# Kernel optimization log

Measured on AMD Instinct MI355X. Metric: run time of the kernel, lower is better.

## Reference

```python
import jax, jax.numpy as jnp
import numpy as np

N, F_IN, HID, C, E = 100000, 1024, 16, 64, 3200000
BN_EPS = 1e-5


def setup_inputs() -> dict:
    key = jax.random.key(0)
    ks = jax.random.split(key, 8)
    x = jax.random.normal(ks[0], (N, F_IN), jnp.float32)
    edge_index = jax.random.randint(ks[1], (2, E), 0, N, dtype=jnp.int32)
    w1 = jax.random.normal(ks[2], (F_IN, HID), jnp.float32) / np.float32(np.sqrt(F_IN))
    b1 = jnp.zeros((HID,), jnp.float32)
    w2 = jax.random.normal(ks[3], (HID, C), jnp.float32) / np.float32(np.sqrt(HID))
    b2 = jnp.zeros((C,), jnp.float32)
    mlp_w = jax.random.normal(ks[4], (C, C), jnp.float32) / np.float32(np.sqrt(C))
    mlp_b = jnp.zeros((C,), jnp.float32)
    bn_gamma = jnp.ones((C,), jnp.float32)
    bn_beta = jnp.zeros((C,), jnp.float32)
    # per-node channel weight param, xavier_normal_ init on shape (N, 1)
    xavier_std = np.float32(np.sqrt(2.0 / (N + 1)))
    weight_raw = jax.random.normal(ks[5], (N, 1), jnp.float32) * xavier_std
    return {"x": x, "edge_index": edge_index, "w1": w1, "b1": b1, "w2": w2,
            "b2": b2, "mlp_w": mlp_w, "mlp_b": mlp_b, "bn_gamma": bn_gamma,
            "bn_beta": bn_beta, "weight_raw": weight_raw}


def _gcn_norm(edge_index, n):
    # PyG GCNConv default: add self-loops, norm = deg^-1/2[src] * deg^-1/2[dst]
    loop = jnp.arange(n, dtype=edge_index.dtype)
    src = jnp.concatenate([edge_index[0], loop])
    dst = jnp.concatenate([edge_index[1], loop])
    deg = jax.ops.segment_sum(jnp.ones_like(dst, dtype=jnp.float32), dst, num_segments=n)
    dis = jax.lax.rsqrt(jnp.maximum(deg, 1.0))  # deg >= 1 with self-loops
    norm = dis[src] * dis[dst]
    return src, dst, norm


def _gcn_conv(h, src, dst, norm, w, b, n):
    h = h @ w                              # [N, out] dense transform first
    msg = h[src] * norm[:, None]           # gather + scale per edge
    out = jax.ops.segment_sum(msg, dst, num_segments=n)  # scatter-add
    return out + b


def reference(x, edge_index, w1, b1, w2, b2, mlp_w, mlp_b, bn_gamma, bn_beta, weight_raw):
    n = x.shape[0]
    src, dst, norm = _gcn_norm(edge_index, n)
    h = _gcn_conv(x, src, dst, norm, w1, b1, n)
    h = jax.nn.relu(h)                     # dropout is identity in eval mode
    h = _gcn_conv(h, src, dst, norm, w2, b2, n)
    h = jax.nn.log_softmax(h, axis=1)
    h = jnp.exp(weight_raw) * h            # exp(xavier param) channel weight
    h = h @ mlp_w + mlp_b                  # final MLP (C*1 -> C)
    mean = jnp.mean(h, axis=0)
    var = jnp.mean(jnp.square(h - mean), axis=0)  # biased var, BN training stats
    h = (h - mean) * jax.lax.rsqrt(var + BN_EPS) * bn_gamma + bn_beta
    return jax.nn.log_softmax(h, axis=1)
```

## Files before the change

### kernel.cpp

```cpp
#include <hip/hip_runtime.h>
#include <math.h>

#define NN   100000
#define FIN  1024
#define HIDN 16
#define CCH  64
#define EE   3200000
#define BNEPS 1e-5f
#define NB   ((NN + 255) / 256)
#define NPART 8
#define PSZ  (NN / NPART)

__global__ __launch_bounds__(256) void k_hist(const int* __restrict__ ei,
                                              unsigned* __restrict__ deg) {
  int p = blockIdx.x & 7;
  int blk = blockIdx.x >> 3;
  int nblk = gridDim.x >> 3;
  int lo = p * PSZ, hi = lo + PSZ;
  for (int e = blk * 256 + threadIdx.x; e < EE; e += nblk * 256) {
    int d = ei[EE + e];
    if (d >= lo && d < hi) atomicAdd(&deg[d], 1u);
  }
}

__global__ __launch_bounds__(256) void k_scan_part(const unsigned* __restrict__ deg,
                                                   unsigned* __restrict__ exc,
                                                   unsigned* __restrict__ bsum) {
  __shared__ unsigned s[256];
  int t = threadIdx.x, i = blockIdx.x * 256 + t;
  unsigned v = (i < NN) ? deg[i] : 0u;
  s[t] = v;
  __syncthreads();
#pragma unroll
  for (int off = 1; off < 256; off <<= 1) {
    unsigned u = (t >= off) ? s[t - off] : 0u;
    __syncthreads();
    s[t] += u;
    __syncthreads();
  }
  if (i < NN) exc[i] = s[t] - v;
  if (t == 255) bsum[blockIdx.x] = s[255];
}

__global__ __launch_bounds__(512) void k_scan_boff(const unsigned* __restrict__ bsum,
                                                   unsigned* __restrict__ boff) {
  __shared__ unsigned s[512];
  int t = threadIdx.x;
  unsigned v = (t < NB) ? bsum[t] : 0u;
  s[t] = v;
  __syncthreads();
#pragma unroll
  for (int off = 1; off < 512; off <<= 1) {
    unsigned u = (t >= off) ? s[t - off] : 0u;
    __syncthreads();
    s[t] += u;
    __syncthreads();
  }
  if (t < NB) boff[t] = s[t] - v;
}

__global__ __launch_bounds__(256) void k_scan_final(const unsigned* __restrict__ exc,
                                                    const unsigned* __restrict__ boff,
                                                    const unsigned* __restrict__ deg,
                                                    int* __restrict__ rowptr,
                                                    int* __restrict__ cur,
                                                    float* __restrict__ dis) {
  int i = blockIdx.x * 256 + threadIdx.x;
  if (i < NN) {
    int r = (int)(boff[i >> 8] + exc[i]);
    rowptr[i] = r;
    cur[i] = r;
    dis[i] = rsqrtf((float)(deg[i] + 1u));
  } else if (i == NN) {
    rowptr[NN] = EE;
  }
}

__global__ __launch_bounds__(256) void k_place(const int* __restrict__ ei,
                                               int* __restrict__ cur,
                                               int* __restrict__ perm) {
  int p = blockIdx.x & 7;
  int blk = blockIdx.x >> 3;
  int nblk = gridDim.x >> 3;
  int lo = p * PSZ, hi = lo + PSZ;
  for (int e = blk * 256 + threadIdx.x; e < EE; e += nblk * 256) {
    int d = ei[EE + e];
    if (d >= lo && d < hi) {
      int s = ei[e];
      int slot = atomicAdd(&cur[d], 1);
      perm[slot] = s;
    }
  }
}

#define G1_ROWS_PER_BLOCK 128
__global__ __launch_bounds__(256, 2) void k_gemm1(const float* __restrict__ x,
                                                  const float* __restrict__ w1,
                                                  const float* __restrict__ dis,
                                                  float* __restrict__ xw1s) {
  __shared__ __align__(16) float w1s[1024 * 16];
  const float4* w1v = (const float4*)w1;
  for (int idx = threadIdx.x; idx < 4096; idx += 256) {
    int k = idx >> 2, qj = idx & 3;
    int pq = qj ^ ((k >> 1) & 3);
    *(float4*)&w1s[(k << 4) + (pq << 2)] = w1v[idx];
  }
  __syncthreads();

  const int lane = threadIdx.x & 63;
  const int wave = threadIdx.x >> 6;
  const int sw = (lane >> 1) & 3;
  const int wave_row0 = blockIdx.x * G1_ROWS_PER_BLOCK + wave * 32;

  for (int g = 0; g < 8; ++g) {
    int row0 = wave_row0 + g * 4;
    if (row0 >= NN) break;
    int r0 = row0;
    int r1 = min(row0 + 1, NN - 1);
    int r2 = min(row0 + 2, NN - 1);
    int r3 = min(row0 + 3, NN - 1);

    const float* p0 = x + (size_t)r0 * FIN + lane;
    const float* p1 = x + (size_t)r1 * FIN + lane;
    const float* p2 = x + (size_t)r2 * FIN + lane;
    const float* p3 = x + (size_t)r3 * FIN + lane;

    float xa[16], xb[16], xc[16], xd[16];
#pragma unroll
    for (int i = 0; i < 16; ++i) {
      xa[i] = p0[i * 64];
      xb[i] = p1[i * 64];
      xc[i] = p2[i * 64];
      xd[i] = p3[i * 64];
    }

    float acc[64];
#pragma unroll
    for (int t = 0; t < 64; ++t) acc[t] = 0.0f;

#pragma unroll
    for (int i = 0; i < 16; ++i) {
      const float* wr = &w1s[(i * 64 + lane) << 4];
      float xv0 = xa[i], xv1 = xb[i], xv2 = xc[i], xv3 = xd[i];
#pragma unroll
      for (int q = 0; q < 4; ++q) {
        float4 wq = *(const float4*)(wr + ((q ^ sw) << 2));
        int b = q * 4;
        acc[b + 0]      += xv0 * wq.x;
        acc[b + 1]      += xv0 * wq.y;
        acc[b + 2]      += xv0 * wq.z;
        acc[b + 3]      += xv0 * wq.w;
        acc[16 + b + 0] += xv1 * wq.x;
        acc[16 + b + 1] += xv1 * wq.y;
        acc[16 + b + 2] += xv1 * wq.z;
        acc[16 + b + 3] += xv1 * wq.w;
        acc[32 + b + 0] += xv2 * wq.x;
        acc[32 + b + 1] += xv2 * wq.y;
        acc[32 + b + 2] += xv2 * wq.z;
        acc[32 + b + 3] += xv2 * wq.w;
        acc[48 + b + 0] += xv3 * wq.x;
        acc[48 + b + 1] += xv3 * wq.y;
        acc[48 + b + 2] += xv3 * wq.z;
        acc[48 + b + 3] += xv3 * wq.w;
      }
    }

#pragma unroll
    for (int o = 32; o >= 1; o >>= 1) {
      bool up = (lane & o) != 0;
#pragma unroll
      for (int t = 0; t < o; ++t) {
        float send = up ? acc[t] : acc[t + o];
        float recv = __shfl_xor(send, o, 64);
        float keep = up ? acc[t + o] : acc[t];
        acc[t] = keep + recv;
      }
    }

    int r = lane >> 4, j = lane & 15;
    int grow = row0 + r;
    if (grow < NN) xw1s[grow * HIDN + j] = acc[0] * dis[grow];
  }
}

template <int MODE>
__global__ __launch_bounds__(256) void k_agg(const int* __restrict__ rowptr,
                                             const int* __restrict__ perm,
                                             const float* __restrict__ dis,
                                             const float* __restrict__ sfs,
                                             const float* __restrict__ b1,
                                             float* __restrict__ out) {
  int g = blockIdx.x * 4 + (threadIdx.x >> 6);
  if (g >= NN) return;
  int lane = threadIdx.x & 63;
  int eo = lane >> 4;
  int j = lane & 15;
  int beg = rowptr[g], end = rowptr[g + 1];
  float acc = 0.0f;
  for (int e = beg + eo; e < end; e += 4) {
    int s = perm[e];
    acc += sfs[(size_t)s * HIDN + j];
  }
  acc += __shfl_xor(acc, 16, 64);
  acc += __shfl_xor(acc, 32, 64);
  if (eo == 0) {
    float di = dis[g];
    float v = di * (acc + sfs[(size_t)g * HIDN + j]);
    if (MODE == 0)
      out[(size_t)g * HIDN + j] = fmaxf(v + b1[j], 0.0f) * di;
    else
      out[(size_t)g * HIDN + j] = v;
  }
}

__global__ __launch_bounds__(256) void k_fuse2(const float* __restrict__ agg2,
                                               const float* __restrict__ w2,
                                               const float* __restrict__ b2,
                                               const float* __restrict__ mlpw,
                                               const float* __restrict__ mlpb,
                                               const float* __restrict__ wraw,
                                               float* __restrict__ out,
                                               double* __restrict__ gsum,
                                               double* __restrict__ gsq) {
  __shared__ float w2s[HIDN * CCH];
  __shared__ float mlps[CCH * CCH];
  __shared__ double reds[256];
  __shared__ double redq[256];
  for (int idx = threadIdx.x; idx < HIDN * CCH; idx += 256) w2s[idx] = w2[idx];
  for (int idx = threadIdx.x; idx < CCH * CCH; idx += 256) mlps[idx] = mlpw[idx];
  __syncthreads();

  const int lane = threadIdx.x & 63;
  const int wave = threadIdx.x >> 6;
  const int j = lane;
  const float b2j = b2[j];
  const float mbj = mlpb[j];
  const int gw = blockIdx.x * 4 + wave;
  const int nw = gridDim.x * 4;

  double sum = 0.0, sq = 0.0;
  for (int i = gw; i < NN; i += nw) {
    float av = agg2[(size_t)i * HIDN + (lane & 15)];
    float h2 = b2j;
#pragma unroll
    for (int k = 0; k < HIDN; ++k)
      h2 = fmaf(__shfl(av, k, 64), w2s[k * CCH + j], h2);

    float mx = h2;
#pragma unroll
    for (int o = 32; o >= 1; o >>= 1) mx = fmaxf(mx, __shfl_xor(mx, o, 64));
    float ex = __expf(h2 - mx);
    float se = ex;
#pragma unroll
    for (int o = 32; o >= 1; o >>= 1) se += __shfl_xor(se, o, 64);
    float lsm = h2 - mx - __logf(se);

    float g = __expf(wraw[i]) * lsm;

    float m = mbj;
#pragma unroll
    for (int c = 0; c < CCH; ++c)
      m = fmaf(__shfl(g, c, 64), mlps[c * CCH + j], m);

    out[(size_t)i * CCH + j] = m;
    sum += (double)m;
    sq = fma((double)m, (double)m, sq);
  }

  reds[threadIdx.x] = sum;
  redq[threadIdx.x] = sq;
  __syncthreads();
  if (threadIdx.x < 64) {
    double s = reds[threadIdx.x] + reds[threadIdx.x + 64] +
               reds[threadIdx.x + 128] + reds[threadIdx.x + 192];
    double q = redq[threadIdx.x] + redq[threadIdx.x + 64] +
               redq[threadIdx.x + 128] + redq[threadIdx.x + 192];
    atomicAdd(&gsum[threadIdx.x], s);
    atomicAdd(&gsq[threadIdx.x], q);
  }
}

__global__ void k_stats(const double* __restrict__ gsum,
                        const double* __restrict__ gsq,
                        const float* __restrict__ gamma,
                        const float* __restrict__ beta,
                        float* __restrict__ bnp) {
  int j = threadIdx.x;
  if (j >= CCH) return;
  const double inv_n = 1.0 / (double)NN;
  double mean = gsum[j] * inv_n;
  double var = gsq[j] * inv_n - mean * mean;
  float sc = (float)(rsqrt(var + (double)BNEPS)) * gamma[j];
  bnp[j] = (float)mean;
  bnp[CCH + j] = sc;
  bnp[2 * CCH + j] = beta[j];
}

__global__ __launch_bounds__(256) void k_out(float* __restrict__ out,
                                             const float* __restrict__ bnp) {
  const int lane = threadIdx.x & 63;
  const int wave = threadIdx.x >> 6;
  const int j = lane;
  const float mean = bnp[j];
  const float sc = bnp[CCH + j];
  const float bt = bnp[2 * CCH + j];
  const int gw = blockIdx.x * 4 + wave;
  const int nw = gridDim.x * 4;
  for (int i = gw; i < NN; i += nw) {
    float m = out[(size_t)i * CCH + j];
    float y = fmaf(m - mean, sc, bt);
    float mx = y;
#pragma unroll
    for (int o = 32; o >= 1; o >>= 1) mx = fmaxf(mx, __shfl_xor(mx, o, 64));
    float ex = __expf(y - mx);
    float se = ex;
#pragma unroll
    for (int o = 32; o >= 1; o >>= 1) se += __shfl_xor(se, o, 64);
    out[(size_t)i * CCH + j] = y - mx - __logf(se);
  }
}

extern "C" void kernel_launch(void* const* d_in, const int* in_sizes, int n_in,
                              void* d_out, int out_size, void* d_ws, size_t ws_size,
                              hipStream_t stream) {
  const float* x     = (const float*)d_in[0];
  const int*   ei    = (const int*)d_in[1];
  const float* w1    = (const float*)d_in[2];
  const float* b1    = (const float*)d_in[3];
  const float* w2    = (const float*)d_in[4];
  const float* b2    = (const float*)d_in[5];
  const float* mlpw  = (const float*)d_in[6];
  const float* mlpb  = (const float*)d_in[7];
  const float* gamma = (const float*)d_in[8];
  const float* beta  = (const float*)d_in[9];
  const float* wraw  = (const float*)d_in[10];
  float* out = (float*)d_out;

  char* w = (char*)d_ws;
  size_t off = 0;
  auto take = [&](size_t bytes) -> void* {
    void* p = w + off;
    off = (off + bytes + 255) & ~(size_t)255;
    return p;
  };
  unsigned* deg    = (unsigned*)take((size_t)NN * 4);
  float*    dis    = (float*)take((size_t)NN * 4);
  unsigned* exc    = (unsigned*)take((size_t)NN * 4);
  unsigned* bsum   = (unsigned*)take((size_t)NB * 4);
  unsigned* boff   = (unsigned*)take((size_t)NB * 4);
  int*      rowptr = (int*)take((size_t)(NN + 1) * 4);
  int*      cur    = (int*)take((size_t)NN * 4);
  int*      perm   = (int*)take((size_t)EE * 4);
  float*    xw1s   = (float*)take((size_t)NN * HIDN * 4);
  float*    rh1s   = (float*)take((size_t)NN * HIDN * 4);
  float*    agg2   = (float*)take((size_t)NN * HIDN * 4);
  double*   gsum   = (double*)take(CCH * 8);
  double*   gsq    = (double*)take(CCH * 8);
  float*    bnp    = (float*)take(3 * CCH * 4);
  (void)ws_size; (void)n_in; (void)in_sizes; (void)out_size;

  hipMemsetAsync(deg, 0, (size_t)NN * 4, stream);
  hipMemsetAsync(gsum, 0, CCH * 8, stream);
  hipMemsetAsync(gsq, 0, CCH * 8, stream);

  k_hist<<<2048, 256, 0, stream>>>(ei, deg);
  k_scan_part<<<NB, 256, 0, stream>>>(deg, exc, bsum);
  k_scan_boff<<<1, 512, 0, stream>>>(bsum, boff);
  k_scan_final<<<(NN + 256) / 256 + 1, 256, 0, stream>>>(exc, boff, deg, rowptr, cur, dis);
  k_place<<<2048, 256, 0, stream>>>(ei, cur, perm);

  k_gemm1<<<(NN + G1_ROWS_PER_BLOCK - 1) / G1_ROWS_PER_BLOCK, 256, 0, stream>>>(
      x, w1, dis, xw1s);
  k_agg<0><<<(NN + 3) / 4, 256, 0, stream>>>(rowptr, perm, dis, xw1s, b1, rh1s);
  k_agg<1><<<(NN + 3) / 4, 256, 0, stream>>>(rowptr, perm, dis, rh1s, b1, agg2);
  k_fuse2<<<2048, 256, 0, stream>>>(agg2, w2, b2, mlpw, mlpb, wraw, out, gsum, gsq);
  k_stats<<<1, 64, 0, stream>>>(gsum, gsq, gamma, beta, bnp);
  k_out<<<1024, 256, 0, stream>>>(out, bnp);
}
```

Baseline: 701.3 us.

## Double-buffer x loads in gemm1, unroll aggregation, use LDS broadcast in fuse2

The first GEMM kernel now double-buffers its x row loads in registers, so the next 4-row group is fetched while the current one is computed. The aggregation kernel keeps two accumulators per lane so that two independent gathers are in flight. The fused second stage replaces per-element wave shuffles with LDS broadcast reads of packed float2 weights. The extra 64-float buffer raises register pressure in gemm1, which may spill or cut occupancy. In fuse2, per-wave LDS buffers are written and read without an explicit barrier and rely on wave-synchronous execution.

```diff
diff --git a/kernel.cpp b/kernel.cpp
--- a/kernel.cpp
+++ b/kernel.cpp
@@ -94,6 +94,78 @@
 }
 
 #define G1_ROWS_PER_BLOCK 128
+
+__device__ __forceinline__ void g1_load(const float* __restrict__ x, int row0,
+                                        int lane, float (&buf)[64]) {
+  int r0 = min(row0,     NN - 1);
+  int r1 = min(row0 + 1, NN - 1);
+  int r2 = min(row0 + 2, NN - 1);
+  int r3 = min(row0 + 3, NN - 1);
+  const float* p0 = x + (size_t)r0 * FIN + lane;
+  const float* p1 = x + (size_t)r1 * FIN + lane;
+  const float* p2 = x + (size_t)r2 * FIN + lane;
+  const float* p3 = x + (size_t)r3 * FIN + lane;
+#pragma unroll
+  for (int i = 0; i < 16; ++i) {
+    buf[i]      = p0[i * 64];
+    buf[16 + i] = p1[i * 64];
+    buf[32 + i] = p2[i * 64];
+    buf[48 + i] = p3[i * 64];
+  }
+}
+
+__device__ __forceinline__ void g1_compute_store(const float (&buf)[64],
+                                                 const float* w1s, int row0,
+                                                 int lane, int sw,
+                                                 const float* __restrict__ dis,
+                                                 float* __restrict__ xw1s) {
+  float acc[64];
+#pragma unroll
+  for (int t = 0; t < 64; ++t) acc[t] = 0.0f;
+
+#pragma unroll
+  for (int i = 0; i < 16; ++i) {
+    const float* wr = &w1s[(i * 64 + lane) << 4];
+    float xv0 = buf[i], xv1 = buf[16 + i], xv2 = buf[32 + i], xv3 = buf[48 + i];
+#pragma unroll
+    for (int q = 0; q < 4; ++q) {
+      float4 wq = *(const float4*)(wr + ((q ^ sw) << 2));
+      int b = q * 4;
+      acc[b + 0]      += xv0 * wq.x;
+      acc[b + 1]      += xv0 * wq.y;
+      acc[b + 2]      += xv0 * wq.z;
+      acc[b + 3]      += xv0 * wq.w;
+      acc[16 + b + 0] += xv1 * wq.x;
+      acc[16 + b + 1] += xv1 * wq.y;
+      acc[16 + b + 2] += xv1 * wq.z;
+      acc[16 + b + 3] += xv1 * wq.w;
+      acc[32 + b + 0] += xv2 * wq.x;
+      acc[32 + b + 1] += xv2 * wq.y;
+      acc[32 + b + 2] += xv2 * wq.z;
+      acc[32 + b + 3] += xv2 * wq.w;
+      acc[48 + b + 0] += xv3 * wq.x;
+      acc[48 + b + 1] += xv3 * wq.y;
+      acc[48 + b + 2] += xv3 * wq.z;
+      acc[48 + b + 3] += xv3 * wq.w;
+    }
+  }
+
+#pragma unroll
+  for (int o = 32; o >= 1; o >>= 1) {
+    bool up = (lane & o) != 0;
+#pragma unroll
+    for (int t = 0; t < o; ++t) {
+      float send = up ? acc[t] : acc[t + o];
+      float recv = __shfl_xor(send, o, 64);
+      float keep = up ? acc[t + o] : acc[t];
+      acc[t] = keep + recv;
+    }
+  }
+
+  int grow = row0 + (lane >> 4);
+  if (grow < NN) xw1s[grow * HIDN + (lane & 15)] = acc[0] * dis[grow];
+}
+
 __global__ __launch_bounds__(256, 2) void k_gemm1(const float* __restrict__ x,
                                                   const float* __restrict__ w1,
                                                   const float* __restrict__ dis,
@@ -112,74 +184,16 @@
   const int sw = (lane >> 1) & 3;
   const int wave_row0 = blockIdx.x * G1_ROWS_PER_BLOCK + wave * 32;
 
-  for (int g = 0; g < 8; ++g) {
-    int row0 = wave_row0 + g * 4;
-    if (row0 >= NN) break;
-    int r0 = row0;
-    int r1 = min(row0 + 1, NN - 1);
-    int r2 = min(row0 + 2, NN - 1);
-    int r3 = min(row0 + 3, NN - 1);
-
-    const float* p0 = x + (size_t)r0 * FIN + lane;
-    const float* p1 = x + (size_t)r1 * FIN + lane;
-    const float* p2 = x + (size_t)r2 * FIN + lane;
-    const float* p3 = x + (size_t)r3 * FIN + lane;
-
-    float xa[16], xb[16], xc[16], xd[16];
-#pragma unroll
-    for (int i = 0; i < 16; ++i) {
-      xa[i] = p0[i * 64];
-      xb[i] = p1[i * 64];
-      xc[i] = p2[i * 64];
-      xd[i] = p3[i * 64];
-    }
-
-    float acc[64];
-#pragma unroll
-    for (int t = 0; t < 64; ++t) acc[t] = 0.0f;
-
-#pragma unroll
-    for (int i = 0; i < 16; ++i) {
-      const float* wr = &w1s[(i * 64 + lane) << 4];
-      float xv0 = xa[i], xv1 = xb[i], xv2 = xc[i], xv3 = xd[i];
-#pragma unroll
-      for (int q = 0; q < 4; ++q) {
-        float4 wq = *(const float4*)(wr + ((q ^ sw) << 2));
-        int b = q * 4;
-        acc[b + 0]      += xv0 * wq.x;
-        acc[b + 1]      += xv0 * wq.y;
-        acc[b + 2]      += xv0 * wq.z;
-        acc[b + 3]      += xv0 * wq.w;
-        acc[16 + b + 0] += xv1 * wq.x;
-        acc[16 + b + 1] += xv1 * wq.y;
-        acc[16 + b + 2] += xv1 * wq.z;
-        acc[16 + b + 3] += xv1 * wq.w;
-        acc[32 + b + 0] += xv2 * wq.x;
-        acc[32 + b + 1] += xv2 * wq.y;
-        acc[32 + b + 2] += xv2 * wq.z;
-        acc[32 + b + 3] += xv2 * wq.w;
-        acc[48 + b + 0] += xv3 * wq.x;
-        acc[48 + b + 1] += xv3 * wq.y;
-        acc[48 + b + 2] += xv3 * wq.z;
-        acc[48 + b + 3] += xv3 * wq.w;
-      }
-    }
-
-#pragma unroll
-    for (int o = 32; o >= 1; o >>= 1) {
-      bool up = (lane & o) != 0;
-#pragma unroll
-      for (int t = 0; t < o; ++t) {
-        float send = up ? acc[t] : acc[t + o];
-        float recv = __shfl_xor(send, o, 64);
-        float keep = up ? acc[t + o] : acc[t];
-        acc[t] = keep + recv;
-      }
-    }
-
-    int r = lane >> 4, j = lane & 15;
-    int grow = row0 + r;
-    if (grow < NN) xw1s[grow * HIDN + j] = acc[0] * dis[grow];
+  float bufA[64], bufB[64];
+  g1_load(x, wave_row0, lane, bufA);
+
+  for (int gg = 0; gg < 4; ++gg) {
+    int r_even = wave_row0 + (2 * gg) * 4;
+    int r_odd  = wave_row0 + (2 * gg + 1) * 4;
+    g1_load(x, r_odd, lane, bufB);
+    g1_compute_store(bufA, w1s, r_even, lane, sw, dis, xw1s);
+    if (gg < 3) g1_load(x, wave_row0 + (2 * gg + 2) * 4, lane, bufA);
+    g1_compute_store(bufB, w1s, r_odd, lane, sw, dis, xw1s);
   }
 }
 
@@ -196,11 +210,16 @@
   int eo = lane >> 4;
   int j = lane & 15;
   int beg = rowptr[g], end = rowptr[g + 1];
-  float acc = 0.0f;
-  for (int e = beg + eo; e < end; e += 4) {
-    int s = perm[e];
-    acc += sfs[(size_t)s * HIDN + j];
-  }
+  float acc0 = 0.0f, acc1 = 0.0f;
+  int e = beg + eo;
+  for (; e + 4 < end; e += 8) {
+    int s0 = perm[e];
+    int s1 = perm[e + 4];
+    acc0 += sfs[(size_t)s0 * HIDN + j];
+    acc1 += sfs[(size_t)s1 * HIDN + j];
+  }
+  if (e < end) acc0 += sfs[(size_t)perm[e] * HIDN + j];
+  float acc = acc0 + acc1;
   acc += __shfl_xor(acc, 16, 64);
   acc += __shfl_xor(acc, 32, 64);
   if (eo == 0) {
@@ -222,12 +241,20 @@
                                                float* __restrict__ out,
                                                double* __restrict__ gsum,
                                                double* __restrict__ gsq) {
-  __shared__ float w2s[HIDN * CCH];
-  __shared__ float mlps[CCH * CCH];
+  __shared__ __align__(16) float2 w2p[8 * CCH];
+  __shared__ __align__(16) float2 mlpp[32 * CCH];
+  __shared__ __align__(16) float avbuf[4][HIDN];
+  __shared__ __align__(16) float gbuf[4][CCH];
   __shared__ double reds[256];
   __shared__ double redq[256];
-  for (int idx = threadIdx.x; idx < HIDN * CCH; idx += 256) w2s[idx] = w2[idx];
-  for (int idx = threadIdx.x; idx < CCH * CCH; idx += 256) mlps[idx] = mlpw[idx];
+  for (int idx = threadIdx.x; idx < 8 * CCH; idx += 256) {
+    int k2 = idx >> 6, j = idx & 63;
+    w2p[idx] = make_float2(w2[(2 * k2) * CCH + j], w2[(2 * k2 + 1) * CCH + j]);
+  }
+  for (int idx = threadIdx.x; idx < 32 * CCH; idx += 256) {
+    int c2 = idx >> 6, j = idx & 63;
+    mlpp[idx] = make_float2(mlpw[(2 * c2) * CCH + j], mlpw[(2 * c2 + 1) * CCH + j]);
+  }
   __syncthreads();
 
   const int lane = threadIdx.x & 63;
@@ -241,10 +268,17 @@
   double sum = 0.0, sq = 0.0;
   for (int i = gw; i < NN; i += nw) {
     float av = agg2[(size_t)i * HIDN + (lane & 15)];
-    float h2 = b2j;
-#pragma unroll
-    for (int k = 0; k < HIDN; ++k)
-      h2 = fmaf(__shfl(av, k, 64), w2s[k * CCH + j], h2);
+    if (lane < HIDN) avbuf[wave][lane] = av;
+
+    float2 h2p = make_float2(0.0f, 0.0f);
+#pragma unroll
+    for (int k2 = 0; k2 < 8; ++k2) {
+      float2 a = *(const float2*)&avbuf[wave][2 * k2];
+      float2 wv = w2p[k2 * CCH + j];
+      h2p.x = fmaf(a.x, wv.x, h2p.x);
+      h2p.y = fmaf(a.y, wv.y, h2p.y);
+    }
+    float h2 = h2p.x + h2p.y + b2j;
 
     float mx = h2;
 #pragma unroll
@@ -255,12 +289,18 @@
     for (int o = 32; o >= 1; o >>= 1) se += __shfl_xor(se, o, 64);
     float lsm = h2 - mx - __logf(se);
 
-    float g = __expf(wraw[i]) * lsm;
-
-    float m = mbj;
-#pragma unroll
-    for (int c = 0; c < CCH; ++c)
-      m = fmaf(__shfl(g, c, 64), mlps[c * CCH + j], m);
+    float gg = __expf(wraw[i]) * lsm;
+    gbuf[wave][j] = gg;
+
+    float2 mp = make_float2(0.0f, 0.0f);
+#pragma unroll
+    for (int c2 = 0; c2 < 32; ++c2) {
+      float2 gv = *(const float2*)&gbuf[wave][2 * c2];
+      float2 wv = mlpp[c2 * CCH + j];
+      mp.x = fmaf(gv.x, wv.x, mp.x);
+      mp.y = fmaf(gv.y, wv.y, mp.y);
+    }
+    float m = mp.x + mp.y + mbj;
 
     out[(size_t)i * CCH + j] = m;
     sum += (double)m;
```

New measurement: 1.536 ms. 2.19x slower.
